# Kernel tuning notes

Measured on AMD Instinct MI355X. Metric: run time of the kernel, lower is better.

The kernel has to match this reference:

```python
import jax, jax.numpy as jnp
import numpy as np

DIM = 512
HEADS = 8
HEAD_DIM = DIM // HEADS
SCALING = float(np.sqrt(HEAD_DIM))
B, S = 8, 2048


def setup_inputs() -> dict:
    key = jax.random.key(0)
    ks = jax.random.split(key, 6)
    x = jax.random.normal(ks[0], (B, S, DIM), dtype=jnp.float32)
    mask = jax.random.randint(ks[1], (B, S), 0, 2).astype(bool)
    mask = mask.at[:, 0].set(False)  # guarantee at least one unmasked key per row
    lim_qkv = 1.0 / np.sqrt(DIM)
    Wqkv = jax.random.uniform(ks[2], (3 * DIM, DIM), minval=-lim_qkv, maxval=lim_qkv, dtype=jnp.float32)
    bqkv = jax.random.uniform(ks[3], (3 * DIM,), minval=-lim_qkv, maxval=lim_qkv, dtype=jnp.float32)
    Wout = jax.random.uniform(ks[4], (DIM, DIM), minval=-lim_qkv, maxval=lim_qkv, dtype=jnp.float32)
    bout = jax.random.uniform(ks[5], (DIM,), minval=-lim_qkv, maxval=lim_qkv, dtype=jnp.float32)
    ln_g = jnp.ones((DIM,), dtype=jnp.float32)
    ln_b = jnp.zeros((DIM,), dtype=jnp.float32)
    return {"x": x, "mask": mask, "Wqkv": Wqkv, "bqkv": bqkv, "Wout": Wout, "bout": bout, "ln_g": ln_g, "ln_b": ln_b}


def reference(x, mask, Wqkv, bqkv, Wout, bout, ln_g, ln_b):
    b, s, _ = x.shape
    qkv = x @ Wqkv.T + bqkv                                   # [b, s, 3*dim]
    qkv = qkv.reshape(b, s, HEADS, HEAD_DIM, 3)               # torch reshape semantics (interleaved)
    q = qkv[..., 0]                                           # [b, s, h, d]
    k = qkv[..., 1]
    v = jax.nn.elu(qkv[..., 2])
    attn = jnp.einsum('bqhd,bkhd->bhqk', q, k) / SCALING      # [b, h, s, s]
    bias = jnp.where(mask[:, None, None, :], -jnp.inf, 0.0).astype(attn.dtype)
    attn = jax.nn.softmax(attn + bias, axis=-1)
    out = jnp.einsum('bhqk,bkhd->bqhd', attn, v).reshape(b, s, DIM)
    out = out @ Wout.T + bout
    mu = jnp.mean(out, axis=-1, keepdims=True)
    var = jnp.var(out, axis=-1, keepdims=True)
    out = (out - mu) / jnp.sqrt(var + 1e-5) * ln_g + ln_b
    return jax.nn.elu(out)
```

## Files before the change

### kernel.cpp

```cpp
#include <hip/hip_runtime.h>

#define DIM 512
#define HEADS 8
#define HD 64
#define NB 8
#define NS 2048
#define SCALE_INV 0.125f
#define C2F 0.18033688011112042f
#define NEG_BIG -1e30f
#define QSZ 8388608

typedef __attribute__((ext_vector_type(8))) short bf16x8;
typedef __attribute__((ext_vector_type(4))) float f32x4;

__device__ __forceinline__ float elu_f(float x) {
    return x > 0.0f ? x : (__expf(x) - 1.0f);
}
__device__ __forceinline__ short f2bf(float x) {
    union { float f; unsigned u; } v; v.f = x;
    unsigned r = v.u + 0x7FFFu + ((v.u >> 16) & 1u);
    return (short)(r >> 16);
}
__device__ __forceinline__ float exp2_hw(float x) {
    float r; asm("v_exp_f32 %0, %1" : "=v"(r) : "v"(x)); return r;
}
__device__ __forceinline__ unsigned cvt_pk_bf16(float a, float b) {
    unsigned r; asm("v_cvt_pk_bf16_f32 %0, %1, %2" : "=v"(r) : "v"(a), "v"(b)); return r;
}

__device__ __forceinline__ void gload16(const void* g, void* l) {
    __builtin_amdgcn_global_load_lds(
        (const __attribute__((address_space(1))) unsigned*)g,
        (__attribute__((address_space(3))) unsigned*)l, 16, 0, 0);
}
__device__ __forceinline__ void gload4(const void* g, void* l) {
    __builtin_amdgcn_global_load_lds(
        (const __attribute__((address_space(1))) unsigned*)g,
        (__attribute__((address_space(3))) unsigned*)l, 4, 0, 0);
}

#define X4 2097152
#define W14 196608
#define W24 65536
__global__ __launch_bounds__(256) void prep(
    const float* __restrict__ x, const float* __restrict__ Wqkv,
    const float* __restrict__ bqkv, const float* __restrict__ Wout,
    const int* __restrict__ mask,
    short* __restrict__ xb, short* __restrict__ Wp,
    float* __restrict__ bp, short* __restrict__ Wob,
    float* __restrict__ maskf)
{
    int i = blockIdx.x * 256 + threadIdx.x;
    if (i < X4) {
        float4 v = *(const float4*)(x + (size_t)i * 4);
        ushort4 o; o.x = (unsigned short)f2bf(v.x); o.y = (unsigned short)f2bf(v.y);
        o.z = (unsigned short)f2bf(v.z); o.w = (unsigned short)f2bf(v.w);
        *(ushort4*)(xb + (size_t)i * 4) = o;
    } else if (i < X4 + W14) {
        int j = i - X4;
        int np = j >> 7, k = (j & 127) * 4;
        int w = np >> 9, h = (np >> 6) & 7, d = np & 63;
        int n = h * 192 + d * 3 + w;
        float4 v = *(const float4*)(Wqkv + (size_t)n * 512 + k);
        ushort4 o; o.x = (unsigned short)f2bf(v.x); o.y = (unsigned short)f2bf(v.y);
        o.z = (unsigned short)f2bf(v.z); o.w = (unsigned short)f2bf(v.w);
        *(ushort4*)(Wp + (size_t)np * 512 + k) = o;
    } else if (i < X4 + W14 + W24) {
        int j = i - X4 - W14;
        float4 v = *(const float4*)(Wout + (size_t)j * 4);
        ushort4 o; o.x = (unsigned short)f2bf(v.x); o.y = (unsigned short)f2bf(v.y);
        o.z = (unsigned short)f2bf(v.z); o.w = (unsigned short)f2bf(v.w);
        *(ushort4*)(Wob + (size_t)j * 4) = o;
    } else if (i < X4 + W14 + W24 + 1536) {
        int j = i - X4 - W14 - W24;
        int w = j >> 9, h = (j >> 6) & 7, d = j & 63;
        bp[j] = bqkv[h * 192 + d * 3 + w];
    } else {
        int j = i - X4 - W14 - W24 - 1536;
        maskf[j] = mask[j] ? NEG_BIG : 0.0f;
    }
}

__global__ __launch_bounds__(256) void qkv_mfma(
    const short* __restrict__ A, const short* __restrict__ Bw,
    const float* __restrict__ bp, short* __restrict__ QKV)
{
    __shared__ short smem[2 * 128 * 64];
    short* As = smem;
    short* Bs = smem + 128 * 64;
    const int t = threadIdx.x, lane = t & 63, wv = t >> 6;
    const int c = lane & 15, quad = lane >> 4;
    const int wr = wv >> 1, wc = wv & 1;
    const int rsub = lane >> 3;
    const int csA = (lane & 7) ^ rsub;
    const int m0 = blockIdx.x * 128, n0 = blockIdx.y * 128;
    f32x4 acc[4][4];
    #pragma unroll
    for (int mi = 0; mi < 4; ++mi)
        #pragma unroll
        for (int nj = 0; nj < 4; ++nj)
            #pragma unroll
            for (int i = 0; i < 4; ++i) acc[mi][nj][i] = 0.0f;

    for (int k0 = 0; k0 < 512; k0 += 64) {
        if (k0) __syncthreads();
        #pragma unroll
        for (int p = 0; p < 4; ++p) {
            int r = p * 32 + wv * 8 + rsub;
            gload16(A  + (size_t)(m0 + r) * 512 + k0 + csA * 8, &As[(p * 4 + wv) * 512]);
            gload16(Bw + (size_t)(n0 + r) * 512 + k0 + csA * 8, &Bs[(p * 4 + wv) * 512]);
        }
        __syncthreads();
        bf16x8 af[4][2], bfr[4][2];
        #pragma unroll
        for (int mi = 0; mi < 4; ++mi) {
            int ar = wr * 64 + mi * 16 + c;
            af[mi][0] = *(const bf16x8*)&As[ar * 64 + ((quad       ^ (ar & 7)) * 8)];
            af[mi][1] = *(const bf16x8*)&As[ar * 64 + (((4 + quad) ^ (ar & 7)) * 8)];
        }
        #pragma unroll
        for (int nj = 0; nj < 4; ++nj) {
            int br = wc * 64 + nj * 16 + c;
            bfr[nj][0] = *(const bf16x8*)&Bs[br * 64 + ((quad       ^ (br & 7)) * 8)];
            bfr[nj][1] = *(const bf16x8*)&Bs[br * 64 + (((4 + quad) ^ (br & 7)) * 8)];
        }
        __builtin_amdgcn_s_setprio(1);
        #pragma unroll
        for (int mi = 0; mi < 4; ++mi)
            #pragma unroll
            for (int nj = 0; nj < 4; ++nj) {
                acc[mi][nj] = __builtin_amdgcn_mfma_f32_16x16x32_bf16(af[mi][0], bfr[nj][0], acc[mi][nj], 0, 0, 0);
                acc[mi][nj] = __builtin_amdgcn_mfma_f32_16x16x32_bf16(af[mi][1], bfr[nj][1], acc[mi][nj], 0, 0, 0);
            }
        __builtin_amdgcn_s_setprio(0);
    }

    const int w  = n0 >> 9;
    const int b  = m0 >> 11;
    const int hh = ((n0 + wc * 64) >> 6) & 7;
    float bv[4];
    #pragma unroll
    for (int nj = 0; nj < 4; ++nj) bv[nj] = bp[n0 + wc * 64 + nj * 16 + c];

    if (w < 2) {
        short* out = QKV + (size_t)w * QSZ + (size_t)(b * 8 + hh) * NS * 64;
        #pragma unroll
        for (int mi = 0; mi < 4; ++mi)
            #pragma unroll
            for (int i = 0; i < 4; ++i) {
                int s = (m0 & (NS - 1)) + wr * 64 + mi * 16 + quad * 4 + i;
                #pragma unroll
                for (int nj = 0; nj < 4; ++nj)
                    out[(size_t)s * 64 + nj * 16 + c] = f2bf(acc[mi][nj][i] + bv[nj]);
            }
    } else {
        __syncthreads();
        short* T = smem;
        #pragma unroll
        for (int mi = 0; mi < 4; ++mi)
            #pragma unroll
            for (int i = 0; i < 4; ++i) {
                int ml = wr * 64 + mi * 16 + quad * 4 + i;
                int mb = ml >> 3, mr = ml & 7;
                #pragma unroll
                for (int nj = 0; nj < 4; ++nj) {
                    int nl = wc * 64 + nj * 16 + c;
                    T[nl * 128 + ((mb ^ (nl & 15)) * 8) + mr] =
                        f2bf(elu_f(acc[mi][nj][i] + bv[nj]));
                }
            }
        __syncthreads();
        short* Vt = QKV + (size_t)2 * QSZ;
        #pragma unroll
        for (int p = 0; p < 8; ++p) {
            int idx = p * 256 + t, row = idx >> 4, ch = idx & 15;
            uint4 v = *(const uint4*)&T[row * 128 + ((ch ^ (row & 15)) * 8)];
            int d = row & 63;
            int h2 = ((n0 + row) >> 6) & 7;
            int sg = (m0 & (NS - 1)) + ch * 8;
            int kt = sg >> 6, ks = sg & 63;
            *(uint4*)(Vt + (((size_t)(b * 8 + h2) * 32 + kt) * 64 + d) * 64 + ks) = v;
        }
    }
}

__global__ __launch_bounds__(512, 4) void attn_mfma(
    const short* __restrict__ Qg, const short* __restrict__ Kg,
    const short* __restrict__ Vg, const float* __restrict__ maskf,
    short* __restrict__ O)
{
    __shared__ short Pt[128 * 64];
    __shared__ short Ks[2][64 * 64];
    __shared__ short Vs[2][64 * 64];
    __shared__ float msk[2][64];
    __shared__ float lw[128];

    const int t = threadIdx.x;
    const int lane = t & 63;
    const int wv = t >> 6;
    const int wq = wv & 3;
    const int wk = wv >> 2;
    const int c = lane & 15;
    const int quad = lane >> 4;
    const int bid = blockIdx.x;
    const int qt = bid & 15;
    const int h  = (bid >> 4) & 7;
    const int b  = bid >> 7;
    const int g  = b * 8 + h;
    const size_t base = (size_t)g * NS * HD;
    const int q0 = qt * 128;

    const int rsub = lane >> 3;
    const int csA  = (lane & 7) ^ rsub;
    const int csV  = ((lane & 7) - rsub) & 7;

    #pragma unroll
    for (int p = 0; p < 2; ++p) {
        int r = wv * 16 + p * 8 + rsub;
        gload16(Qg + base + (size_t)(q0 + r) * HD + csA * 8, &Pt[(wv * 2 + p) * 512]);
    }
    {
        int r = wv * 8 + rsub;
        gload16(Kg + base + (size_t)r * HD + csA * 8, &Ks[0][wv * 512]);
        gload16(Vg + (((size_t)g * 32 + 0) * 64 + r) * 64 + csV * 8, &Vs[0][wv * 512]);
        if (wv == 0) gload4(maskf + (size_t)b * NS + lane, &msk[0][0]);
    }
    __syncthreads();

    bf16x8 bq[2][2];
    #pragma unroll
    for (int nj = 0; nj < 2; ++nj) {
        int mq = wq * 32 + nj * 16 + c;
        bq[nj][0] = *(const bf16x8*)&Pt[mq * 64 + ((quad       ^ (mq & 7)) * 8)];
        bq[nj][1] = *(const bf16x8*)&Pt[mq * 64 + (((4 + quad) ^ (mq & 7)) * 8)];
    }
    __syncthreads();

    {
        int r = wv * 8 + rsub;
        gload16(Kg + base + (size_t)(64 + r) * HD + csA * 8, &Ks[1][wv * 512]);
        gload16(Vg + (((size_t)g * 32 + 1) * 64 + r) * 64 + csV * 8, &Vs[1][wv * 512]);
        if (wv == 0) gload4(maskf + (size_t)b * NS + 64 + lane, &msk[1][0]);
    }

    bf16x8 onesA;
    #pragma unroll
    for (int i = 0; i < 8; ++i) onesA[i] = (short)0x3F80;

    f32x4 o[4][2];
    #pragma unroll
    for (int dc = 0; dc < 4; ++dc)
        #pragma unroll
        for (int nj = 0; nj < 2; ++nj)
            #pragma unroll
            for (int i = 0; i < 4; ++i) o[dc][nj][i] = 0.0f;
    f32x4 lacc[2];
    #pragma unroll
    for (int nj = 0; nj < 2; ++nj)
        #pragma unroll
        for (int i = 0; i < 4; ++i) lacc[nj][i] = 0.0f;

    const int prot  = 8 * (c & 7);
    const int kbase = wk * 32;

    for (int kt = 0; kt < 32; ++kt) {
        const int cur = kt & 1;
        const short* Kc = Ks[cur];
        const short* Vc = Vs[cur];

        f32x4 st[2][2];
        __builtin_amdgcn_s_setprio(1);
        #pragma unroll
        for (int ks = 0; ks < 2; ++ks) {
            int kr = kbase + ks * 16 + c;
            bf16x8 ak0 = *(const bf16x8*)&Kc[kr * 64 + ((quad       ^ (kr & 7)) * 8)];
            bf16x8 ak1 = *(const bf16x8*)&Kc[kr * 64 + (((4 + quad) ^ (kr & 7)) * 8)];
            #pragma unroll
            for (int nj = 0; nj < 2; ++nj) {
                f32x4 a = {0.0f, 0.0f, 0.0f, 0.0f};
                a = __builtin_amdgcn_mfma_f32_16x16x32_bf16(ak0, bq[nj][0], a, 0, 0, 0);
                a = __builtin_amdgcn_mfma_f32_16x16x32_bf16(ak1, bq[nj][1], a, 0, 0, 0);
                st[ks][nj] = a;
            }
        }
        __builtin_amdgcn_s_setprio(0);

        #pragma unroll
        for (int ks = 0; ks < 2; ++ks) {
            float4 mb = *(const float4*)&msk[cur][kbase + ks * 16 + quad * 4];
            #pragma unroll
            for (int nj = 0; nj < 2; ++nj) {
                float p0 = exp2_hw(st[ks][nj][0] * C2F + mb.x);
                float p1 = exp2_hw(st[ks][nj][1] * C2F + mb.y);
                float p2 = exp2_hw(st[ks][nj][2] * C2F + mb.z);
                float p3 = exp2_hw(st[ks][nj][3] * C2F + mb.w);
                uint2 pk;
                pk.x = cvt_pk_bf16(p0, p1);
                pk.y = cvt_pk_bf16(p2, p3);
                *(uint2*)&Pt[(wq * 32 + nj * 16 + c) * 64 +
                             ((kbase + ks * 16 + quad * 4 + prot) & 63)] = pk;
            }
        }

        bf16x8 bp[2];
        #pragma unroll
        for (int nj = 0; nj < 2; ++nj)
            bp[nj] = *(const bf16x8*)&Pt[(wq * 32 + nj * 16 + c) * 64 +
                                         ((kbase + quad * 8 + prot) & 63)];

        __builtin_amdgcn_s_setprio(1);
        #pragma unroll
        for (int nj = 0; nj < 2; ++nj)
            lacc[nj] = __builtin_amdgcn_mfma_f32_16x16x32_bf16(onesA, bp[nj], lacc[nj], 0, 0, 0);
        #pragma unroll
        for (int dc = 0; dc < 4; ++dc) {
            int d = dc * 16 + c;
            int vrot = 8 * (d & 7);
            bf16x8 av = *(const bf16x8*)&Vc[d * 64 + ((kbase + quad * 8 + vrot) & 63)];
            #pragma unroll
            for (int nj = 0; nj < 2; ++nj)
                o[dc][nj] = __builtin_amdgcn_mfma_f32_16x16x32_bf16(av, bp[nj], o[dc][nj], 0, 0, 0);
        }
        __builtin_amdgcn_s_setprio(0);

        __syncthreads();

        if (kt + 2 < 32) {
            int r = wv * 8 + rsub;
            int k0n = (kt + 2) * 64;
            gload16(Kg + base + (size_t)(k0n + r) * HD + csA * 8, &Ks[cur][wv * 512]);
            gload16(Vg + (((size_t)g * 32 + (kt + 2)) * 64 + r) * 64 + csV * 8, &Vs[cur][wv * 512]);
            if (wv == 0) gload4(maskf + (size_t)b * NS + k0n + lane, &msk[cur][0]);
        }
    }

    float* rb = ((wq < 2) ? (float*)&Ks[0][0] : (float*)&Vs[0][0])
                + (wq & 1) * 2048 + lane * 32;
    if (wk == 1) {
        #pragma unroll
        for (int dc = 0; dc < 4; ++dc)
            #pragma unroll
            for (int nj = 0; nj < 2; ++nj)
                *(f32x4*)&rb[(((dc << 1) | nj) ^ (lane & 7)) << 2] = o[dc][nj];
        if (quad == 0) {
            lw[wq * 32 + c]      = lacc[0][0];
            lw[wq * 32 + 16 + c] = lacc[1][0];
        }
    }
    __syncthreads();
    if (wk == 0) {
        float l0 = lacc[0][0] + lw[wq * 32 + c];
        float l1 = lacc[1][0] + lw[wq * 32 + 16 + c];
        float inv0 = 1.0f / l0;
        float inv1 = 1.0f / l1;
        #pragma unroll
        for (int dc = 0; dc < 4; ++dc)
            #pragma unroll
            for (int nj = 0; nj < 2; ++nj)
                o[dc][nj] += *(const f32x4*)&rb[(((dc << 1) | nj) ^ (lane & 7)) << 2];
        #pragma unroll
        for (int nj = 0; nj < 2; ++nj) {
            float inv = nj ? inv1 : inv0;
            int q = q0 + wq * 32 + nj * 16 + c;
            short* orow = O + ((size_t)(b * NS + q)) * DIM + h * HD + quad * 4;
            #pragma unroll
            for (int dc = 0; dc < 4; ++dc) {
                uint2 pk;
                pk.x = (unsigned)(unsigned short)f2bf(o[dc][nj][0] * inv)
                     | ((unsigned)(unsigned short)f2bf(o[dc][nj][1] * inv) << 16);
                pk.y = (unsigned)(unsigned short)f2bf(o[dc][nj][2] * inv)
                     | ((unsigned)(unsigned short)f2bf(o[dc][nj][3] * inv) << 16);
                *(uint2*)(orow + dc * 16) = pk;
            }
        }
    }
}

__global__ __launch_bounds__(256) void out_mfma(
    const short* __restrict__ A, const short* __restrict__ Bw,
    const float* __restrict__ bias, float* __restrict__ Z)
{
    __shared__ short smem[2 * 128 * 64];
    short* As = smem;
    short* Bs = smem + 128 * 64;
    const int t = threadIdx.x, lane = t & 63, wv = t >> 6;
    const int c = lane & 15, quad = lane >> 4;
    const int wr = wv >> 1, wc = wv & 1;
    const int rsub = lane >> 3;
    const int csA = (lane & 7) ^ rsub;
    const int m0 = blockIdx.x * 128, n0 = blockIdx.y * 128;
    f32x4 acc[4][4];
    #pragma unroll
    for (int mi = 0; mi < 4; ++mi)
        #pragma unroll
        for (int nj = 0; nj < 4; ++nj)
            #pragma unroll
            for (int i = 0; i < 4; ++i) acc[mi][nj][i] = 0.0f;

    for (int k0 = 0; k0 < 512; k0 += 64) {
        if (k0) __syncthreads();
        #pragma unroll
        for (int p = 0; p < 4; ++p) {
            int r = p * 32 + wv * 8 + rsub;
            gload16(A  + (size_t)(m0 + r) * 512 + k0 + csA * 8, &As[(p * 4 + wv) * 512]);
            gload16(Bw + (size_t)(n0 + r) * 512 + k0 + csA * 8, &Bs[(p * 4 + wv) * 512]);
        }
        __syncthreads();
        bf16x8 af[4][2], bfr[4][2];
        #pragma unroll
        for (int mi = 0; mi < 4; ++mi) {
            int ar = wr * 64 + mi * 16 + c;
            af[mi][0] = *(const bf16x8*)&As[ar * 64 + ((quad       ^ (ar & 7)) * 8)];
            af[mi][1] = *(const bf16x8*)&As[ar * 64 + (((4 + quad) ^ (ar & 7)) * 8)];
        }
        #pragma unroll
        for (int nj = 0; nj < 4; ++nj) {
            int br = wc * 64 + nj * 16 + c;
            bfr[nj][0] = *(const bf16x8*)&Bs[br * 64 + ((quad       ^ (br & 7)) * 8)];
            bfr[nj][1] = *(const bf16x8*)&Bs[br * 64 + (((4 + quad) ^ (br & 7)) * 8)];
        }
        __builtin_amdgcn_s_setprio(1);
        #pragma unroll
        for (int mi = 0; mi < 4; ++mi)
            #pragma unroll
            for (int nj = 0; nj < 4; ++nj) {
                acc[mi][nj] = __builtin_amdgcn_mfma_f32_16x16x32_bf16(af[mi][0], bfr[nj][0], acc[mi][nj], 0, 0, 0);
                acc[mi][nj] = __builtin_amdgcn_mfma_f32_16x16x32_bf16(af[mi][1], bfr[nj][1], acc[mi][nj], 0, 0, 0);
            }
        __builtin_amdgcn_s_setprio(0);
    }
    #pragma unroll
    for (int mi = 0; mi < 4; ++mi)
        #pragma unroll
        for (int i = 0; i < 4; ++i) {
            int mrow = m0 + wr * 64 + mi * 16 + quad * 4 + i;
            #pragma unroll
            for (int nj = 0; nj < 4; ++nj) {
                int n = n0 + wc * 64 + nj * 16 + c;
                Z[(size_t)mrow * 512 + n] = acc[mi][nj][i] + bias[n];
            }
        }
}

__global__ __launch_bounds__(256) void ln_elu(
    const float* __restrict__ Z, const float* __restrict__ g,
    const float* __restrict__ bt, float* __restrict__ out)
{
    const int row = blockIdx.x;
    const float* z = Z + (size_t)row * DIM;
    const int t = threadIdx.x;
    float v0 = z[t], v1 = z[t + 256];
    float s  = v0 + v1;
    float ss = v0 * v0 + v1 * v1;
    #pragma unroll
    for (int off = 32; off > 0; off >>= 1) {
        s  += __shfl_down(s, off);
        ss += __shfl_down(ss, off);
    }
    __shared__ float rs[4], rss[4];
    int wid = t >> 6, lane = t & 63;
    if (lane == 0) { rs[wid] = s; rss[wid] = ss; }
    __syncthreads();
    float S1 = rs[0] + rs[1] + rs[2] + rs[3];
    float S2 = rss[0] + rss[1] + rss[2] + rss[3];
    float mu  = S1 * (1.0f / DIM);
    float var = S2 * (1.0f / DIM) - mu * mu;
    float rstd = rsqrtf(var + 1e-5f);
    float y0 = (v0 - mu) * rstd * g[t]       + bt[t];
    float y1 = (v1 - mu) * rstd * g[t + 256] + bt[t + 256];
    out[(size_t)row * DIM + t]       = elu_f(y0);
    out[(size_t)row * DIM + t + 256] = elu_f(y1);
}

extern "C" void kernel_launch(void* const* d_in, const int* in_sizes, int n_in,
                              void* d_out, int out_size, void* d_ws, size_t ws_size,
                              hipStream_t stream)
{
    const float* x    = (const float*)d_in[0];
    const int*   mask = (const int*)d_in[1];
    const float* Wqkv = (const float*)d_in[2];
    const float* bqkv = (const float*)d_in[3];
    const float* Wout = (const float*)d_in[4];
    const float* bout = (const float*)d_in[5];
    const float* ln_g = (const float*)d_in[6];
    const float* ln_b = (const float*)d_in[7];
    float* out = (float*)d_out;

    short* xb   = (short*)d_ws;
    short* Wp   = xb + QSZ;
    short* Wob  = Wp + 786432;
    short* QKV  = Wob + 262144;
    short* ATTb = QKV + 3 * (size_t)QSZ;
    float* bp   = (float*)(ATTb + QSZ);
    float* Zb   = bp + 1536;
    float* maskf = Zb + (size_t)QSZ - 16384;

    prep<<<9286, 256, 0, stream>>>(x, Wqkv, bqkv, Wout, mask, xb, Wp, bp, Wob, maskf);
    qkv_mfma<<<dim3(128, 12), 256, 0, stream>>>(xb, Wp, bp, QKV);
    attn_mfma<<<1024, 512, 0, stream>>>(QKV, QKV + QSZ, QKV + 2 * (size_t)QSZ, maskf, ATTb);
    out_mfma<<<dim3(128, 4), 256, 0, stream>>>(ATTb, Wob, bout, Zb);
    ln_elu<<<NB * NS, 256, 0, stream>>>(Zb, ln_g, ln_b, out);
}
```

Baseline: 238.6 us.

## Load V fragments directly from global into registers, drop V LDS staging

V tiles are no longer staged through double-buffered shared memory. Each lane now reads its MFMA A-operand fragment straight from global memory, with the next tile prefetched into registers after each barrier. The row-sum MFMA against a ones vector is replaced by scalar fp32 accumulation of the probabilities plus a cross-quad shuffle reduction. The smaller LDS footprint allows launch bounds to raise occupancy from 4 to 6 blocks. The risks are exposed global-load latency on the V operand and more register pressure, and the row sum now uses unrounded fp32 probabilities while the PV product uses bf16.

```diff
diff --git a/kernel.cpp b/kernel.cpp
--- a/kernel.cpp
+++ b/kernel.cpp
@@ -184,14 +184,13 @@
     }
 }
 
-__global__ __launch_bounds__(512, 4) void attn_mfma(
+__global__ __launch_bounds__(512, 6) void attn_mfma(
     const short* __restrict__ Qg, const short* __restrict__ Kg,
     const short* __restrict__ Vg, const float* __restrict__ maskf,
     short* __restrict__ O)
 {
     __shared__ short Pt[128 * 64];
     __shared__ short Ks[2][64 * 64];
-    __shared__ short Vs[2][64 * 64];
     __shared__ float msk[2][64];
     __shared__ float lw[128];
 
@@ -212,7 +211,9 @@
 
     const int rsub = lane >> 3;
     const int csA  = (lane & 7) ^ rsub;
-    const int csV  = ((lane & 7) - rsub) & 7;
+
+    const int kbase = wk * 32;
+    const short* vfb = Vg + (size_t)g * 32 * 4096 + (size_t)c * 64 + kbase + quad * 8;
 
     #pragma unroll
     for (int p = 0; p < 2; ++p) {
@@ -222,7 +223,6 @@
     {
         int r = wv * 8 + rsub;
         gload16(Kg + base + (size_t)r * HD + csA * 8, &Ks[0][wv * 512]);
-        gload16(Vg + (((size_t)g * 32 + 0) * 64 + r) * 64 + csV * 8, &Vs[0][wv * 512]);
         if (wv == 0) gload4(maskf + (size_t)b * NS + lane, &msk[0][0]);
     }
     __syncthreads();
@@ -236,17 +236,15 @@
     }
     __syncthreads();
 
+    bf16x8 av[4];
+    #pragma unroll
+    for (int dc = 0; dc < 4; ++dc) av[dc] = *(const bf16x8*)(vfb + dc * 1024);
     {
         int r = wv * 8 + rsub;
         gload16(Kg + base + (size_t)(64 + r) * HD + csA * 8, &Ks[1][wv * 512]);
-        gload16(Vg + (((size_t)g * 32 + 1) * 64 + r) * 64 + csV * 8, &Vs[1][wv * 512]);
         if (wv == 0) gload4(maskf + (size_t)b * NS + 64 + lane, &msk[1][0]);
     }
 
-    bf16x8 onesA;
-    #pragma unroll
-    for (int i = 0; i < 8; ++i) onesA[i] = (short)0x3F80;
-
     f32x4 o[4][2];
     #pragma unroll
     for (int dc = 0; dc < 4; ++dc)
@@ -254,19 +252,13 @@
         for (int nj = 0; nj < 2; ++nj)
             #pragma unroll
             for (int i = 0; i < 4; ++i) o[dc][nj][i] = 0.0f;
-    f32x4 lacc[2];
-    #pragma unroll
-    for (int nj = 0; nj < 2; ++nj)
-        #pragma unroll
-        for (int i = 0; i < 4; ++i) lacc[nj][i] = 0.0f;
-
-    const int prot  = 8 * (c & 7);
-    const int kbase = wk * 32;
+    float lp[2] = {0.0f, 0.0f};
+
+    const int prot = 8 * (c & 7);
 
     for (int kt = 0; kt < 32; ++kt) {
         const int cur = kt & 1;
         const short* Kc = Ks[cur];
-        const short* Vc = Vs[cur];
 
         f32x4 st[2][2];
         __builtin_amdgcn_s_setprio(1);
@@ -294,6 +286,7 @@
                 float p1 = exp2_hw(st[ks][nj][1] * C2F + mb.y);
                 float p2 = exp2_hw(st[ks][nj][2] * C2F + mb.z);
                 float p3 = exp2_hw(st[ks][nj][3] * C2F + mb.w);
+                lp[nj] += (p0 + p1) + (p2 + p3);
                 uint2 pk;
                 pk.x = cvt_pk_bf16(p0, p1);
                 pk.y = cvt_pk_bf16(p2, p3);
@@ -310,31 +303,34 @@
 
         __builtin_amdgcn_s_setprio(1);
         #pragma unroll
-        for (int nj = 0; nj < 2; ++nj)
-            lacc[nj] = __builtin_amdgcn_mfma_f32_16x16x32_bf16(onesA, bp[nj], lacc[nj], 0, 0, 0);
-        #pragma unroll
-        for (int dc = 0; dc < 4; ++dc) {
-            int d = dc * 16 + c;
-            int vrot = 8 * (d & 7);
-            bf16x8 av = *(const bf16x8*)&Vc[d * 64 + ((kbase + quad * 8 + vrot) & 63)];
+        for (int dc = 0; dc < 4; ++dc)
             #pragma unroll
             for (int nj = 0; nj < 2; ++nj)
-                o[dc][nj] = __builtin_amdgcn_mfma_f32_16x16x32_bf16(av, bp[nj], o[dc][nj], 0, 0, 0);
-        }
+                o[dc][nj] = __builtin_amdgcn_mfma_f32_16x16x32_bf16(av[dc], bp[nj], o[dc][nj], 0, 0, 0);
         __builtin_amdgcn_s_setprio(0);
 
         __syncthreads();
 
+        if (kt + 1 < 32) {
+            const short* vb = vfb + (size_t)(kt + 1) * 4096;
+            #pragma unroll
+            for (int dc = 0; dc < 4; ++dc) av[dc] = *(const bf16x8*)(vb + dc * 1024);
+        }
         if (kt + 2 < 32) {
             int r = wv * 8 + rsub;
             int k0n = (kt + 2) * 64;
             gload16(Kg + base + (size_t)(k0n + r) * HD + csA * 8, &Ks[cur][wv * 512]);
-            gload16(Vg + (((size_t)g * 32 + (kt + 2)) * 64 + r) * 64 + csV * 8, &Vs[cur][wv * 512]);
             if (wv == 0) gload4(maskf + (size_t)b * NS + k0n + lane, &msk[cur][0]);
         }
     }
 
-    float* rb = ((wq < 2) ? (float*)&Ks[0][0] : (float*)&Vs[0][0])
+    #pragma unroll
+    for (int nj = 0; nj < 2; ++nj) {
+        lp[nj] += __shfl_xor(lp[nj], 16);
+        lp[nj] += __shfl_xor(lp[nj], 32);
+    }
+
+    float* rb = ((wq < 2) ? (float*)&Ks[0][0] : (float*)&Pt[0])
                 + (wq & 1) * 2048 + lane * 32;
     if (wk == 1) {
         #pragma unroll
@@ -343,14 +339,14 @@
             for (int nj = 0; nj < 2; ++nj)
                 *(f32x4*)&rb[(((dc << 1) | nj) ^ (lane & 7)) << 2] = o[dc][nj];
         if (quad == 0) {
-            lw[wq * 32 + c]      = lacc[0][0];
-            lw[wq * 32 + 16 + c] = lacc[1][0];
+            lw[wq * 32 + c]      = lp[0];
+            lw[wq * 32 + 16 + c] = lp[1];
         }
     }
     __syncthreads();
     if (wk == 0) {
-        float l0 = lacc[0][0] + lw[wq * 32 + c];
-        float l1 = lacc[1][0] + lw[wq * 32 + 16 + c];
+        float l0 = lp[0] + lw[wq * 32 + c];
+        float l1 = lp[1] + lw[wq * 32 + 16 + c];
         float inv0 = 1.0f / l0;
         float inv1 = 1.0f / l1;
         #pragma unroll
```

Measured after the change: 751.9 us. 215% more time.

## Fuse output projection with LayerNorm and ELU in one full-row GEMM kernel

Applied to the files above, without the earlier changes.

Replaces the separate output-projection GEMM and LayerNorm+ELU kernels with one kernel. Each block computes a 64-row by 512-column tile so it holds whole rows. It then does the row mean and variance reduction with shuffles and shared memory, and writes the normalized ELU output directly. This removes the fp32 intermediate Z write and read and one kernel launch. In exchange, the grid shrinks to 256 blocks with larger shared-memory tiles (64 KB for B), which may reduce occupancy and parallelism.

```diff
diff --git a/kernel.cpp b/kernel.cpp
--- a/kernel.cpp
+++ b/kernel.cpp
@@ -376,100 +376,106 @@
     }
 }
 
-__global__ __launch_bounds__(256) void out_mfma(
+__global__ __launch_bounds__(512) void out_ln(
     const short* __restrict__ A, const short* __restrict__ Bw,
-    const float* __restrict__ bias, float* __restrict__ Z)
+    const float* __restrict__ bias, const float* __restrict__ g,
+    const float* __restrict__ bt, float* __restrict__ out)
 {
-    __shared__ short smem[2 * 128 * 64];
-    short* As = smem;
-    short* Bs = smem + 128 * 64;
+    __shared__ short As[64 * 64];
+    __shared__ short Bs[512 * 64];
     const int t = threadIdx.x, lane = t & 63, wv = t >> 6;
     const int c = lane & 15, quad = lane >> 4;
-    const int wr = wv >> 1, wc = wv & 1;
+    const int wr = wv >> 2, wc = wv & 3;
     const int rsub = lane >> 3;
     const int csA = (lane & 7) ^ rsub;
-    const int m0 = blockIdx.x * 128, n0 = blockIdx.y * 128;
-    f32x4 acc[4][4];
-    #pragma unroll
-    for (int mi = 0; mi < 4; ++mi)
-        #pragma unroll
-        for (int nj = 0; nj < 4; ++nj)
+    const int m0 = blockIdx.x * 64;
+
+    float bv[8], gg[8], bb[8];
+    #pragma unroll
+    for (int nj = 0; nj < 8; ++nj) {
+        int col = wc * 128 + nj * 16 + c;
+        bv[nj] = bias[col]; gg[nj] = g[col]; bb[nj] = bt[col];
+    }
+
+    f32x4 acc[2][8];
+    #pragma unroll
+    for (int mi = 0; mi < 2; ++mi)
+        #pragma unroll
+        for (int nj = 0; nj < 8; ++nj)
             #pragma unroll
             for (int i = 0; i < 4; ++i) acc[mi][nj][i] = 0.0f;
 
     for (int k0 = 0; k0 < 512; k0 += 64) {
         if (k0) __syncthreads();
-        #pragma unroll
-        for (int p = 0; p < 4; ++p) {
-            int r = p * 32 + wv * 8 + rsub;
-            gload16(A  + (size_t)(m0 + r) * 512 + k0 + csA * 8, &As[(p * 4 + wv) * 512]);
-            gload16(Bw + (size_t)(n0 + r) * 512 + k0 + csA * 8, &Bs[(p * 4 + wv) * 512]);
+        gload16(A + (size_t)(m0 + wv * 8 + rsub) * 512 + k0 + csA * 8, &As[wv * 512]);
+        #pragma unroll
+        for (int p = 0; p < 8; ++p) {
+            int r = p * 64 + wv * 8 + rsub;
+            gload16(Bw + (size_t)r * 512 + k0 + csA * 8, &Bs[(p * 8 + wv) * 512]);
         }
         __syncthreads();
-        bf16x8 af[4][2], bfr[4][2];
-        #pragma unroll
-        for (int mi = 0; mi < 4; ++mi) {
-            int ar = wr * 64 + mi * 16 + c;
+        bf16x8 af[2][2];
+        #pragma unroll
+        for (int mi = 0; mi < 2; ++mi) {
+            int ar = wr * 32 + mi * 16 + c;
             af[mi][0] = *(const bf16x8*)&As[ar * 64 + ((quad       ^ (ar & 7)) * 8)];
             af[mi][1] = *(const bf16x8*)&As[ar * 64 + (((4 + quad) ^ (ar & 7)) * 8)];
         }
-        #pragma unroll
-        for (int nj = 0; nj < 4; ++nj) {
-            int br = wc * 64 + nj * 16 + c;
-            bfr[nj][0] = *(const bf16x8*)&Bs[br * 64 + ((quad       ^ (br & 7)) * 8)];
-            bfr[nj][1] = *(const bf16x8*)&Bs[br * 64 + (((4 + quad) ^ (br & 7)) * 8)];
-        }
         __builtin_amdgcn_s_setprio(1);
         #pragma unroll
-        for (int mi = 0; mi < 4; ++mi)
-            #pragma unroll
-            for (int nj = 0; nj < 4; ++nj) {
-                acc[mi][nj] = __builtin_amdgcn_mfma_f32_16x16x32_bf16(af[mi][0], bfr[nj][0], acc[mi][nj], 0, 0, 0);
-                acc[mi][nj] = __builtin_amdgcn_mfma_f32_16x16x32_bf16(af[mi][1], bfr[nj][1], acc[mi][nj], 0, 0, 0);
-            }
+        for (int nj = 0; nj < 8; ++nj) {
+            int br = wc * 128 + nj * 16 + c;
+            bf16x8 b0 = *(const bf16x8*)&Bs[br * 64 + ((quad       ^ (br & 7)) * 8)];
+            bf16x8 b1 = *(const bf16x8*)&Bs[br * 64 + (((4 + quad) ^ (br & 7)) * 8)];
+            #pragma unroll
+            for (int mi = 0; mi < 2; ++mi) {
+                acc[mi][nj] = __builtin_amdgcn_mfma_f32_16x16x32_bf16(af[mi][0], b0, acc[mi][nj], 0, 0, 0);
+                acc[mi][nj] = __builtin_amdgcn_mfma_f32_16x16x32_bf16(af[mi][1], b1, acc[mi][nj], 0, 0, 0);
+            }
+        }
         __builtin_amdgcn_s_setprio(0);
     }
-    #pragma unroll
-    for (int mi = 0; mi < 4; ++mi)
+    __syncthreads();
+
+    float* red = (float*)As;
+    #pragma unroll
+    for (int mi = 0; mi < 2; ++mi)
         #pragma unroll
         for (int i = 0; i < 4; ++i) {
-            int mrow = m0 + wr * 64 + mi * 16 + quad * 4 + i;
-            #pragma unroll
-            for (int nj = 0; nj < 4; ++nj) {
-                int n = n0 + wc * 64 + nj * 16 + c;
-                Z[(size_t)mrow * 512 + n] = acc[mi][nj][i] + bias[n];
-            }
-        }
-}
-
-__global__ __launch_bounds__(256) void ln_elu(
-    const float* __restrict__ Z, const float* __restrict__ g,
-    const float* __restrict__ bt, float* __restrict__ out)
-{
-    const int row = blockIdx.x;
-    const float* z = Z + (size_t)row * DIM;
-    const int t = threadIdx.x;
-    float v0 = z[t], v1 = z[t + 256];
-    float s  = v0 + v1;
-    float ss = v0 * v0 + v1 * v1;
-    #pragma unroll
-    for (int off = 32; off > 0; off >>= 1) {
-        s  += __shfl_down(s, off);
-        ss += __shfl_down(ss, off);
-    }
-    __shared__ float rs[4], rss[4];
-    int wid = t >> 6, lane = t & 63;
-    if (lane == 0) { rs[wid] = s; rss[wid] = ss; }
+            float s = 0.0f, ss = 0.0f;
+            #pragma unroll
+            for (int nj = 0; nj < 8; ++nj) {
+                float z = acc[mi][nj][i] + bv[nj];
+                s += z; ss += z * z;
+            }
+            s  += __shfl_xor(s, 1);  s  += __shfl_xor(s, 2);
+            s  += __shfl_xor(s, 4);  s  += __shfl_xor(s, 8);
+            ss += __shfl_xor(ss, 1); ss += __shfl_xor(ss, 2);
+            ss += __shfl_xor(ss, 4); ss += __shfl_xor(ss, 8);
+            if (c == 0) {
+                int row = wr * 32 + mi * 16 + quad * 4 + i;
+                red[wc * 64 + row]       = s;
+                red[256 + wc * 64 + row] = ss;
+            }
+        }
     __syncthreads();
-    float S1 = rs[0] + rs[1] + rs[2] + rs[3];
-    float S2 = rss[0] + rss[1] + rss[2] + rss[3];
-    float mu  = S1 * (1.0f / DIM);
-    float var = S2 * (1.0f / DIM) - mu * mu;
-    float rstd = rsqrtf(var + 1e-5f);
-    float y0 = (v0 - mu) * rstd * g[t]       + bt[t];
-    float y1 = (v1 - mu) * rstd * g[t + 256] + bt[t + 256];
-    out[(size_t)row * DIM + t]       = elu_f(y0);
-    out[(size_t)row * DIM + t + 256] = elu_f(y1);
+    #pragma unroll
+    for (int mi = 0; mi < 2; ++mi)
+        #pragma unroll
+        for (int i = 0; i < 4; ++i) {
+            int row = wr * 32 + mi * 16 + quad * 4 + i;
+            float S1 = red[row] + red[64 + row] + red[128 + row] + red[192 + row];
+            float S2 = red[256 + row] + red[320 + row] + red[384 + row] + red[448 + row];
+            float mu   = S1 * (1.0f / DIM);
+            float var  = S2 * (1.0f / DIM) - mu * mu;
+            float rstd = rsqrtf(var + 1e-5f);
+            float* orow = out + (size_t)(m0 + row) * DIM + wc * 128 + c;
+            #pragma unroll
+            for (int nj = 0; nj < 8; ++nj) {
+                float z = acc[mi][nj][i] + bv[nj];
+                orow[nj * 16] = elu_f((z - mu) * rstd * gg[nj] + bb[nj]);
+            }
+        }
 }
 
 extern "C" void kernel_launch(void* const* d_in, const int* in_sizes, int n_in,
@@ -498,6 +504,5 @@
     prep<<<9286, 256, 0, stream>>>(x, Wqkv, bqkv, Wout, mask, xb, Wp, bp, Wob, maskf);
     qkv_mfma<<<dim3(128, 12), 256, 0, stream>>>(xb, Wp, bp, QKV);
     attn_mfma<<<1024, 512, 0, stream>>>(QKV, QKV + QSZ, QKV + 2 * (size_t)QSZ, maskf, ATTb);
-    out_mfma<<<dim3(128, 4), 256, 0, stream>>>(ATTb, Wob, bout, Zb);
-    ln_elu<<<NB * NS, 256, 0, stream>>>(Zb, ln_g, ln_b, out);
-}
+    out_ln<<<256, 512, 0, stream>>>(ATTb, Wob, bout, ln_g, ln_b, out);
+}
```

Measured after the change: 245.5 us. +2.9%, slower.
